# Kernel optimization log

Measured on AMD Instinct MI355X. Metric: run time of the kernel, lower is better.

## Reference

```python
import jax, jax.numpy as jnp
import numpy as np

NUM_CLASSES = 10
N = 1_000_000
D = 128


def setup_inputs() -> dict:
    key = jax.random.key(0)
    k1, k2 = jax.random.split(key)
    x = jax.random.normal(k1, (N, D), dtype=jnp.float32)
    t = jax.random.randint(k2, (N,), 0, NUM_CLASSES, dtype=jnp.int32)
    return {"x": x, "t": t}


def reference(x, t):
    # trace(cov(class_j)) == sum over features of unbiased per-feature variance.
    # Computed as a segment reduction over classes: O(N*D) instead of O(N*D^2).
    nc = NUM_CLASSES
    ones = jnp.ones((x.shape[0],), dtype=x.dtype)
    counts = jax.ops.segment_sum(ones, t, num_segments=nc)            # [C]
    sums = jax.ops.segment_sum(x, t, num_segments=nc)                 # [C, D]
    means = sums / counts[:, None]                                    # [C, D]
    centered = x - means[t]                                           # [N, D]
    sumsq = jax.ops.segment_sum(centered * centered, t, num_segments=nc)  # [C, D]
    trace_per_class = sumsq.sum(axis=1) / (counts - 1.0)              # [C] unbiased (n-1)
    vc = trace_per_class.sum()
    penalty1 = vc / nc
    return jnp.reshape(penalty1, (1,))
```

## Files before the change

kernel.cpp:

```cpp
#include <hip/hip_runtime.h>


#define NCLS 10
#define DFEAT 128
#define NB 1024
#define BLK 256
#define NGRP (NB * (BLK / 32))
#define COLS (NCLS * 130)

__global__ __launch_bounds__(BLK) void k_partial(const float* __restrict__ x,
                                                 const int* __restrict__ t,
                                                 float* __restrict__ partial,
                                                 int N) {
    const int tid = threadIdx.x;
    const int lane32 = tid & 31;
    const int group = blockIdx.x * (BLK / 32) + (tid >> 5);
    const float4* __restrict__ xv = (const float4*)x;

    float4 s[NCLS];
    float sq[NCLS], cn[NCLS];
#pragma unroll
    for (int c = 0; c < NCLS; ++c) {
        s[c] = make_float4(0.f, 0.f, 0.f, 0.f);
        sq[c] = 0.f;
        cn[c] = 0.f;
    }

    for (int row = group; row < N; row += NGRP) {
        float4 v = xv[row * 32 + lane32];
        int cls = t[row];
        float d2 = v.x * v.x + v.y * v.y + v.z * v.z + v.w * v.w;
#pragma unroll
        for (int c = 0; c < NCLS; ++c) {
            if (cls == c) {
                s[c].x += v.x;
                s[c].y += v.y;
                s[c].z += v.z;
                s[c].w += v.w;
                sq[c] += d2;
                cn[c] += 1.0f;
            }
        }
    }

    __shared__ float smem[COLS];
    for (int i = tid; i < COLS; i += BLK) smem[i] = 0.0f;
    __syncthreads();

#pragma unroll
    for (int c = 0; c < NCLS; ++c) {
        atomicAdd(&smem[c * 130 + lane32 * 4 + 0], s[c].x);
        atomicAdd(&smem[c * 130 + lane32 * 4 + 1], s[c].y);
        atomicAdd(&smem[c * 130 + lane32 * 4 + 2], s[c].z);
        atomicAdd(&smem[c * 130 + lane32 * 4 + 3], s[c].w);
        float q = sq[c], n = cn[c];
        for (int off = 16; off > 0; off >>= 1) {
            q += __shfl_down(q, off, 32);
            n += __shfl_down(n, off, 32);
        }
        if (lane32 == 0) {
            atomicAdd(&smem[c * 130 + 128], q);
            atomicAdd(&smem[c * 130 + 129], n);
        }
    }
    __syncthreads();

    for (int i = tid; i < COLS; i += BLK)
        partial[(size_t)i * NB + blockIdx.x] = smem[i];
}

__global__ __launch_bounds__(64) void k_colsum(const float* __restrict__ partial,
                                               float* __restrict__ totals) {
    const int col = blockIdx.x;
    const float* p = partial + (size_t)col * NB;
    float v = 0.f;
    for (int i = threadIdx.x; i < NB; i += 64) v += p[i];
#pragma unroll
    for (int off = 32; off > 0; off >>= 1) v += __shfl_down(v, off, 64);
    if (threadIdx.x == 0) totals[col] = v;
}

__global__ __launch_bounds__(64) void k_final(const float* __restrict__ totals,
                                              float* __restrict__ out) {
    const int lane = threadIdx.x;
    float tr = 0.0f;
    if (lane < NCLS) {
        const float* b = totals + lane * 130;
        float ss = 0.f;
        for (int d = 0; d < DFEAT; ++d) {
            float u = b[d];
            ss += u * u;
        }
        float S2 = b[128];
        float n = b[129] * (1.0f / 32.0f);
        tr = (S2 - ss / n) / (n - 1.0f);
    }
#pragma unroll
    for (int off = 32; off > 0; off >>= 1) tr += __shfl_down(tr, off, 64);
    if (lane == 0) out[0] = tr / (float)NCLS;
}

extern "C" void kernel_launch(void* const* d_in, const int* in_sizes, int n_in,
                              void* d_out, int out_size, void* d_ws, size_t ws_size,
                              hipStream_t stream) {
    const float* x = (const float*)d_in[0];
    const int* t = (const int*)d_in[1];
    const int N = in_sizes[1];

    float* partial = (float*)d_ws;
    float* totals = partial + (size_t)COLS * NB;
    float* out = (float*)d_out;

    k_partial<<<NB, BLK, 0, stream>>>(x, t, partial, N);
    k_colsum<<<COLS, 64, 0, stream>>>(partial, totals);
    k_final<<<1, 64, 0, stream>>>(totals, out);
}
```

Before: 702.6 us.

## Map rows to full 64-lane waves with float2, scalar class, and separate count kernel

```diff
diff --git a/kernel.cpp b/kernel.cpp
--- a/kernel.cpp
+++ b/kernel.cpp
@@ -3,70 +3,72 @@
 
 #define NCLS 10
 #define DFEAT 128
-#define NB 1024
+#define NB 2048
 #define BLK 256
-#define NGRP (NB * (BLK / 32))
-#define COLS (NCLS * 130)
+#define WPB (BLK / 64)
+#define NWAVE (NB * WPB)
+#define CCOLS (NCLS * 129)
+#define CNTB 256
 
-__global__ __launch_bounds__(BLK) void k_partial(const float* __restrict__ x,
-                                                 const int* __restrict__ t,
-                                                 float* __restrict__ partial,
-                                                 int N) {
-    const int tid = threadIdx.x;
-    const int lane32 = tid & 31;
-    const int group = blockIdx.x * (BLK / 32) + (tid >> 5);
-    const float4* __restrict__ xv = (const float4*)x;
+__global__ __launch_bounds__(BLK, 8) void k_partial(const float* __restrict__ x,
+                                                    const int* __restrict__ t,
+                                                    float* __restrict__ partial,
+                                                    int N) {
+    const int lane = threadIdx.x & 63;
+    const int wid = blockIdx.x * WPB + (threadIdx.x >> 6);
+    const float2* __restrict__ xv = (const float2*)x;
 
-    float4 s[NCLS];
-    float sq[NCLS], cn[NCLS];
+    float2 s[NCLS];
+    float sq[NCLS];
 #pragma unroll
     for (int c = 0; c < NCLS; ++c) {
-        s[c] = make_float4(0.f, 0.f, 0.f, 0.f);
+        s[c] = make_float2(0.f, 0.f);
         sq[c] = 0.f;
-        cn[c] = 0.f;
     }
 
-    for (int row = group; row < N; row += NGRP) {
-        float4 v = xv[row * 32 + lane32];
-        int cls = t[row];
-        float d2 = v.x * v.x + v.y * v.y + v.z * v.z + v.w * v.w;
+    for (int r0 = wid * 2; r0 < N; r0 += 2 * NWAVE) {
+        const int r1 = r0 + 1;
+        float2 v0 = xv[(size_t)r0 * 64 + lane];
+        float2 v1 = xv[(size_t)r1 * 64 + lane];
+        const int c0 = __builtin_amdgcn_readfirstlane(t[r0]);
+        const int c1 = __builtin_amdgcn_readfirstlane(t[r1]);
+        const float d0 = v0.x * v0.x + v0.y * v0.y;
+        const float d1 = v1.x * v1.x + v1.y * v1.y;
 #pragma unroll
-        for (int c = 0; c < NCLS; ++c) {
-            if (cls == c) {
-                s[c].x += v.x;
-                s[c].y += v.y;
-                s[c].z += v.z;
-                s[c].w += v.w;
-                sq[c] += d2;
-                cn[c] += 1.0f;
-            }
-        }
+        for (int c = 0; c < NCLS; ++c)
+            if (c0 == c) { s[c].x += v0.x; s[c].y += v0.y; sq[c] += d0; }
+#pragma unroll
+        for (int c = 0; c < NCLS; ++c)
+            if (c1 == c) { s[c].x += v1.x; s[c].y += v1.y; sq[c] += d1; }
     }
 
-    __shared__ float smem[COLS];
-    for (int i = tid; i < COLS; i += BLK) smem[i] = 0.0f;
+    __shared__ float smem[CCOLS];
+    for (int i = threadIdx.x; i < CCOLS; i += BLK) smem[i] = 0.0f;
     __syncthreads();
-
 #pragma unroll
     for (int c = 0; c < NCLS; ++c) {
-        atomicAdd(&smem[c * 130 + lane32 * 4 + 0], s[c].x);
-        atomicAdd(&smem[c * 130 + lane32 * 4 + 1], s[c].y);
-        atomicAdd(&smem[c * 130 + lane32 * 4 + 2], s[c].z);
-        atomicAdd(&smem[c * 130 + lane32 * 4 + 3], s[c].w);
-        float q = sq[c], n = cn[c];
-        for (int off = 16; off > 0; off >>= 1) {
-            q += __shfl_down(q, off, 32);
-            n += __shfl_down(n, off, 32);
-        }
-        if (lane32 == 0) {
-            atomicAdd(&smem[c * 130 + 128], q);
-            atomicAdd(&smem[c * 130 + 129], n);
-        }
+        atomicAdd(&smem[c * 129 + lane * 2 + 0], s[c].x);
+        atomicAdd(&smem[c * 129 + lane * 2 + 1], s[c].y);
+        float q = sq[c];
+#pragma unroll
+        for (int off = 32; off > 0; off >>= 1) q += __shfl_down(q, off, 64);
+        if (lane == 0) atomicAdd(&smem[c * 129 + 128], q);
     }
     __syncthreads();
+    for (int i = threadIdx.x; i < CCOLS; i += BLK)
+        partial[(size_t)i * NB + blockIdx.x] = smem[i];
+}
 
-    for (int i = tid; i < COLS; i += BLK)
-        partial[(size_t)i * NB + blockIdx.x] = smem[i];
+__global__ __launch_bounds__(256) void k_count(const int* __restrict__ t,
+                                               float* __restrict__ countpart, int N) {
+    __shared__ int h[NCLS];
+    if (threadIdx.x < NCLS) h[threadIdx.x] = 0;
+    __syncthreads();
+    for (int i = blockIdx.x * 256 + threadIdx.x; i < N; i += 256 * CNTB)
+        atomicAdd(&h[t[i]], 1);
+    __syncthreads();
+    if (threadIdx.x < NCLS)
+        countpart[threadIdx.x * CNTB + blockIdx.x] = (float)h[threadIdx.x];
 }
 
 __global__ __launch_bounds__(64) void k_colsum(const float* __restrict__ partial,
@@ -81,18 +83,20 @@
 }
 
 __global__ __launch_bounds__(64) void k_final(const float* __restrict__ totals,
+                                              const float* __restrict__ countpart,
                                               float* __restrict__ out) {
     const int lane = threadIdx.x;
     float tr = 0.0f;
     if (lane < NCLS) {
-        const float* b = totals + lane * 130;
+        const float* b = totals + lane * 129;
         float ss = 0.f;
         for (int d = 0; d < DFEAT; ++d) {
             float u = b[d];
             ss += u * u;
         }
-        float S2 = b[128];
-        float n = b[129] * (1.0f / 32.0f);
+        const float S2 = b[128];
+        float n = 0.f;
+        for (int i = 0; i < CNTB; ++i) n += countpart[lane * CNTB + i];
         tr = (S2 - ss / n) / (n - 1.0f);
     }
 #pragma unroll
@@ -108,10 +112,12 @@
     const int N = in_sizes[1];
 
     float* partial = (float*)d_ws;
-    float* totals = partial + (size_t)COLS * NB;
+    float* totals = partial + (size_t)CCOLS * NB;
+    float* countpart = totals + CCOLS;
     float* out = (float*)d_out;
 
     k_partial<<<NB, BLK, 0, stream>>>(x, t, partial, N);
-    k_colsum<<<COLS, 64, 0, stream>>>(partial, totals);
-    k_final<<<1, 64, 0, stream>>>(totals, out);
+    k_count<<<CNTB, 256, 0, stream>>>(t, countpart, N);
+    k_colsum<<<CCOLS, 64, 0, stream>>>(partial, totals);
+    k_final<<<1, 64, 0, stream>>>(totals, countpart, out);
 }
```

After: 717.1 us. +2.1%, slower.
